# Kernel optimization log

Measured on AMD Instinct MI355X. Metric: run time of the kernel, lower is better.

Reference implementation:

```python
import jax, jax.numpy as jnp
import numpy as np

N = 20000      # nodes
E = 640000     # edges
FIN = 256
FQK = 256


def setup_inputs() -> dict:
    key = jax.random.key(0)
    kx, ks, kd, kw = jax.random.split(key, 4)
    x = jax.random.normal(kx, (N, FIN), dtype=jnp.float32)
    # src must be sorted (original scatter_softmax assumes grouped index);
    # force last element to N-1 so nbatches == N as in batch[-1]+1.
    src = jnp.sort(jax.random.randint(ks, (E,), 0, N))
    src = src.at[-1].set(N - 1)
    dest = jax.random.randint(kd, (E,), 0, N)
    ei = jnp.stack([src, dest]).astype(jnp.int64)
    # nn.Linear(Fin, 2*Fqk, bias=False) weight: [2*Fqk, Fin]
    bound = 1.0 / np.sqrt(FIN)
    W = jax.random.uniform(kw, (2 * FQK, FIN), dtype=jnp.float32,
                           minval=-bound, maxval=bound)
    return {"x": x, "ei": ei, "W": W}


def reference(x, ei, W):
    src, dest = ei[0], ei[1]
    n_nodes = x.shape[0]
    scaling = FQK ** -0.5
    qk = x @ W.T                      # [N, 2*Fqk]
    q, k = jnp.split(qk, 2, axis=-1)  # each [N, Fqk]
    q = q * scaling
    # per-edge dot product: (q[src] . k[dest])  -> [E]
    aw = jnp.einsum('ef,ef->e', q[src], k[dest])
    # scatter softmax over edges grouped by src node (raw exp, as original)
    ex = jnp.exp(aw)
    expsum = jax.ops.segment_sum(ex, src, num_segments=n_nodes)  # [N]
    return ex / expsum[src]
```

## Files before the change

kernel.cpp:

```cpp
#include <hip/hip_runtime.h>
#include <cmath>

#define FIN 256
#define FQK 256
#define SCALING 0.0625f
#define MAX_SEG 256

typedef __bf16 bf16_t;
typedef bf16_t bf16x8 __attribute__((ext_vector_type(8)));
typedef float  f32x4  __attribute__((ext_vector_type(4)));

__device__ __forceinline__ unsigned short f2bf(float f) {
    unsigned int u = __float_as_uint(f);
    u += 0x7FFFu + ((u >> 16) & 1u);
    return (unsigned short)(u >> 16);
}
__device__ __forceinline__ float bf_lo(unsigned int w) { return __uint_as_float(w << 16); }
__device__ __forceinline__ float bf_hi(unsigned int w) { return __uint_as_float(w & 0xFFFF0000u); }

__device__ __forceinline__ bf16x8 cvt8(float4 a, float4 b) {
    bf16x8 r;
    r[0] = (bf16_t)a.x; r[1] = (bf16_t)a.y; r[2] = (bf16_t)a.z; r[3] = (bf16_t)a.w;
    r[4] = (bf16_t)b.x; r[5] = (bf16_t)b.y; r[6] = (bf16_t)b.z; r[7] = (bf16_t)b.w;
    return r;
}

__global__ __launch_bounds__(256) void m_seg_kernel(const float* __restrict__ W,
                                                    unsigned short* __restrict__ Mb,
                                                    const int* __restrict__ src,
                                                    int* __restrict__ seg, int N, int E) {
    const int b = blockIdx.x;
    if (b < FIN) {
        const int f = b;
        const int g = threadIdx.x;
        const float* __restrict__ Wq = W;
        const float* __restrict__ Wk = W + FQK * FIN;
        float acc = 0.f;
#pragma unroll 8
        for (int c = 0; c < FQK; ++c)
            acc += Wq[c * FIN + f] * Wk[c * FIN + g];
        Mb[f * FIN + g] = f2bf(acc * SCALING);
    } else {
        const int n = (b - FIN) * 256 + threadIdx.x;
        if (n > N) return;
        int lo = 0, hi = E;
        while (lo < hi) {
            const int mid = (lo + hi) >> 1;
            if (src[mid] < n) lo = mid + 1; else hi = mid;
        }
        seg[n] = lo;
    }
}

__global__ __launch_bounds__(256) void gemm_y_kernel(const float* __restrict__ x,
                                                     const unsigned short* __restrict__ Mb,
                                                     unsigned short* __restrict__ y, int N) {
    const int t    = threadIdx.x;
    const int wv   = t >> 6;
    const int lane = t & 63;
    const int q    = lane >> 4;
    const int m16  = lane & 15;
    const int n0   = blockIdx.x * 16;
    const int f0   = wv * 64;

    const int row  = n0 + m16;
    const int rowc = row < N ? row : N - 1;
    const float* __restrict__ xr = x + (size_t)rowc * FIN;

    f32x4 acc[4] = {};

#pragma unroll
    for (int kc = 0; kc < FIN; kc += 32) {
        const float4 a0 = *(const float4*)(xr + kc + q * 8);
        const float4 a1 = *(const float4*)(xr + kc + q * 8 + 4);
        const bf16x8 af = cvt8(a0, a1);
#pragma unroll
        for (int ft = 0; ft < 4; ++ft) {
            const int f = f0 + ft * 16 + m16;
            union { uint4 u; bf16x8 v; } bu;
            bu.u = *(const uint4*)(Mb + (size_t)f * FIN + kc + q * 8);
            acc[ft] = __builtin_amdgcn_mfma_f32_16x16x32_bf16(af, bu.v, acc[ft], 0, 0, 0);
        }
    }

#pragma unroll
    for (int r = 0; r < 4; ++r) {
        const int n = n0 + q * 4 + r;
        if (n < N) {
#pragma unroll
            for (int ft = 0; ft < 4; ++ft)
                y[(size_t)n * FIN + f0 + ft * 16 + m16] = f2bf(acc[ft][r]);
        }
    }
}

__device__ __forceinline__ float dot8(uint4 qv, float4 xa, float4 xb) {
    return bf_lo(qv.x) * xa.x + bf_hi(qv.x) * xa.y
         + bf_lo(qv.y) * xa.z + bf_hi(qv.y) * xa.w
         + bf_lo(qv.z) * xb.x + bf_hi(qv.z) * xb.y
         + bf_lo(qv.w) * xb.z + bf_hi(qv.w) * xb.w;
}

__global__ __launch_bounds__(256) void node_edge_kernel(const float* __restrict__ x,
                                                        const unsigned short* __restrict__ y,
                                                        const int* __restrict__ dest,
                                                        const int* __restrict__ seg,
                                                        float* __restrict__ out, int N) {
    __shared__ float exlds[4][MAX_SEG];

    const int w    = threadIdx.x >> 6;
    const int lane = threadIdx.x & 63;
    const int n    = blockIdx.x * 4 + w;
    const int g    = lane >> 3;
    const int j    = lane & 7;

    int   s0 = 0, cnt = 0;
    float inv = 0.f;

    if (n < N) {
        s0  = seg[n];
        cnt = seg[n + 1] - s0;
    }

    if (cnt > 0) {
        float4 xf[8];
        const float* __restrict__ xr = x + (size_t)n * FIN + j * 32;
#pragma unroll
        for (int u = 0; u < 8; ++u) xf[u] = *(const float4*)(xr + u * 4);

        float sum = 0.f;
        const int nit = (cnt + 7) >> 3;
        for (int it = 0; it < nit; ++it) {
            const int i = it * 8 + g;
            if (i < cnt) {
                const int d = dest[s0 + i];
                const uint4* __restrict__ yr =
                    (const uint4*)(y + (size_t)d * FIN) + j * 4;
                const uint4 q0 = yr[0];
                const uint4 q1 = yr[1];
                const uint4 q2 = yr[2];
                const uint4 q3 = yr[3];
                float acc = dot8(q0, xf[0], xf[1]) + dot8(q1, xf[2], xf[3])
                          + dot8(q2, xf[4], xf[5]) + dot8(q3, xf[6], xf[7]);
                acc += __shfl_xor(acc, 1, 64);
                acc += __shfl_xor(acc, 2, 64);
                acc += __shfl_xor(acc, 4, 64);
                const float ex = __expf(acc);
                sum += ex;
                if (j == 0 && i < MAX_SEG) exlds[w][i] = ex;
            }
        }
        sum += __shfl_xor(sum, 8, 64);
        sum += __shfl_xor(sum, 16, 64);
        sum += __shfl_xor(sum, 32, 64);
        inv = 1.0f / sum;
    }

    __syncthreads();

    if (cnt > 0) {
        const int lim = cnt < MAX_SEG ? cnt : MAX_SEG;
        for (int i = lane; i < lim; i += 64)
            out[s0 + i] = exlds[w][i] * inv;
    }
}

extern "C" void kernel_launch(void* const* d_in, const int* in_sizes, int n_in,
                              void* d_out, int out_size, void* d_ws, size_t ws_size,
                              hipStream_t stream) {
    const float* x  = (const float*)d_in[0];
    const int*   ei = (const int*)d_in[1];
    const float* W  = (const float*)d_in[2];
    float* out = (float*)d_out;

    const int N = in_sizes[0] / FIN;
    const int E = in_sizes[1] / 2;

    unsigned short* Mb  = (unsigned short*)d_ws;
    unsigned short* y   = Mb + (size_t)FIN * FIN;
    int*            seg = (int*)(y + (size_t)N * FIN);

    const int segBlocks = (N + 256) / 256;
    m_seg_kernel<<<FIN + segBlocks, 256, 0, stream>>>(W, Mb, ei, seg, N, E);

    gemm_y_kernel<<<(N + 15) / 16, 256, 0, stream>>>(x, Mb, y, N);

    node_edge_kernel<<<(N + 3) / 4, 256, 0, stream>>>(x, y, ei + E, seg, out, N);
}
```

Baseline: 160.9 us.

## Pre-swizzle M into MFMA fragment layout, stage x in LDS, prefetch edge rows

M is now written already arranged in MFMA B-fragment order, so each lane's B load in the GEMM is contiguous. The GEMM block grows to 32 rows: x is converted to bf16 once into padded LDS and each B fragment feeds two MFMAs. The edge loop software-pipelines the gather of the next edge's y row while the current dot product is computed, to hide gather latency. In exchange the GEMM uses more LDS and registers and launches fewer blocks, and the prefetch adds register pressure in the edge kernel.

Measured after the change: 137.1 us. 14.8% less time.

```diff
diff --git a/kernel.cpp b/kernel.cpp
--- a/kernel.cpp
+++ b/kernel.cpp
@@ -5,6 +5,7 @@
 #define FQK 256
 #define SCALING 0.0625f
 #define MAX_SEG 256
+#define ASTRIDE 264
 
 typedef __bf16 bf16_t;
 typedef bf16_t bf16x8 __attribute__((ext_vector_type(8)));
@@ -26,20 +27,22 @@
 }
 
 __global__ __launch_bounds__(256) void m_seg_kernel(const float* __restrict__ W,
-                                                    unsigned short* __restrict__ Mb,
+                                                    unsigned short* __restrict__ MbF,
                                                     const int* __restrict__ src,
                                                     int* __restrict__ seg, int N, int E) {
     const int b = blockIdx.x;
     if (b < FIN) {
         const int f = b;
-        const int g = threadIdx.x;
+        const int k = threadIdx.x;
         const float* __restrict__ Wq = W;
         const float* __restrict__ Wk = W + FQK * FIN;
         float acc = 0.f;
 #pragma unroll 8
         for (int c = 0; c < FQK; ++c)
-            acc += Wq[c * FIN + f] * Wk[c * FIN + g];
-        Mb[f * FIN + g] = f2bf(acc * SCALING);
+            acc += Wq[c * FIN + f] * Wk[c * FIN + k];
+        const int ft  = f >> 4, m16 = f & 15;
+        const int kcI = k >> 5, q = (k >> 3) & 3, e = k & 7;
+        MbF[(size_t)(((kcI * 16 + ft) * 64 + q * 16 + m16) * 8 + e)] = f2bf(acc * SCALING);
     } else {
         const int n = (b - FIN) * 256 + threadIdx.x;
         if (n > N) return;
@@ -53,43 +56,66 @@
 }
 
 __global__ __launch_bounds__(256) void gemm_y_kernel(const float* __restrict__ x,
-                                                     const unsigned short* __restrict__ Mb,
+                                                     const unsigned short* __restrict__ MbF,
                                                      unsigned short* __restrict__ y, int N) {
+    __shared__ unsigned short sA[32 * ASTRIDE];
+
     const int t    = threadIdx.x;
     const int wv   = t >> 6;
     const int lane = t & 63;
     const int q    = lane >> 4;
     const int m16  = lane & 15;
-    const int n0   = blockIdx.x * 16;
+    const int n0   = blockIdx.x * 32;
     const int f0   = wv * 64;
 
-    const int row  = n0 + m16;
-    const int rowc = row < N ? row : N - 1;
-    const float* __restrict__ xr = x + (size_t)rowc * FIN;
-
-    f32x4 acc[4] = {};
+    {
+        const int srow = t >> 3;
+        const int scol = (t & 7) * 32;
+        const int n    = n0 + srow;
+        const int nc   = n < N ? n : N - 1;
+        const float* __restrict__ xp = x + (size_t)nc * FIN + scol;
+        unsigned short* __restrict__ sp = &sA[srow * ASTRIDE + scol];
+#pragma unroll
+        for (int u = 0; u < 4; ++u) {
+            const float4 a = *(const float4*)(xp + u * 8);
+            const float4 b = *(const float4*)(xp + u * 8 + 4);
+            *(bf16x8*)(sp + u * 8) = cvt8(a, b);
+        }
+    }
+    __syncthreads();
+
+    f32x4 acc[2][4] = {};
 
 #pragma unroll
     for (int kc = 0; kc < FIN; kc += 32) {
-        const float4 a0 = *(const float4*)(xr + kc + q * 8);
-        const float4 a1 = *(const float4*)(xr + kc + q * 8 + 4);
-        const bf16x8 af = cvt8(a0, a1);
+        bf16x8 afrag[2];
+#pragma unroll
+        for (int mt = 0; mt < 2; ++mt)
+            afrag[mt] = *(const bf16x8*)&sA[(mt * 16 + m16) * ASTRIDE + kc + q * 8];
+
+        const unsigned short* __restrict__ bp =
+            MbF + (size_t)(((kc >> 5) * 16 + (f0 >> 4)) * 64 + lane) * 8;
 #pragma unroll
         for (int ft = 0; ft < 4; ++ft) {
-            const int f = f0 + ft * 16 + m16;
             union { uint4 u; bf16x8 v; } bu;
-            bu.u = *(const uint4*)(Mb + (size_t)f * FIN + kc + q * 8);
-            acc[ft] = __builtin_amdgcn_mfma_f32_16x16x32_bf16(af, bu.v, acc[ft], 0, 0, 0);
-        }
-    }
-
-#pragma unroll
-    for (int r = 0; r < 4; ++r) {
-        const int n = n0 + q * 4 + r;
-        if (n < N) {
-#pragma unroll
-            for (int ft = 0; ft < 4; ++ft)
-                y[(size_t)n * FIN + f0 + ft * 16 + m16] = f2bf(acc[ft][r]);
+            bu.u = *(const uint4*)(bp + ft * 512);
+#pragma unroll
+            for (int mt = 0; mt < 2; ++mt)
+                acc[mt][ft] = __builtin_amdgcn_mfma_f32_16x16x32_bf16(afrag[mt], bu.v,
+                                                                     acc[mt][ft], 0, 0, 0);
+        }
+    }
+
+#pragma unroll
+    for (int mt = 0; mt < 2; ++mt) {
+#pragma unroll
+        for (int r = 0; r < 4; ++r) {
+            const int n = n0 + mt * 16 + q * 4 + r;
+            if (n < N) {
+#pragma unroll
+                for (int ft = 0; ft < 4; ++ft)
+                    y[(size_t)n * FIN + f0 + ft * 16 + m16] = f2bf(acc[mt][ft][r]);
+            }
         }
     }
 }
@@ -130,18 +156,28 @@
 
         float sum = 0.f;
         const int nit = (cnt + 7) >> 3;
+
+        uint4 c0, c1, c2, c3;
+        bool vc = g < cnt;
+        if (vc) {
+            const int d = dest[s0 + g];
+            const uint4* __restrict__ yr = (const uint4*)(y + (size_t)d * FIN) + j * 4;
+            c0 = yr[0]; c1 = yr[1]; c2 = yr[2]; c3 = yr[3];
+        }
+
         for (int it = 0; it < nit; ++it) {
-            const int i = it * 8 + g;
-            if (i < cnt) {
-                const int d = dest[s0 + i];
-                const uint4* __restrict__ yr =
-                    (const uint4*)(y + (size_t)d * FIN) + j * 4;
-                const uint4 q0 = yr[0];
-                const uint4 q1 = yr[1];
-                const uint4 q2 = yr[2];
-                const uint4 q3 = yr[3];
-                float acc = dot8(q0, xf[0], xf[1]) + dot8(q1, xf[2], xf[3])
-                          + dot8(q2, xf[4], xf[5]) + dot8(q3, xf[6], xf[7]);
+            const int i   = it * 8 + g;
+            const int inx = i + 8;
+            const bool vn = inx < cnt;
+            uint4 p0, p1, p2, p3;
+            if (vn) {
+                const int d = dest[s0 + inx];
+                const uint4* __restrict__ yr = (const uint4*)(y + (size_t)d * FIN) + j * 4;
+                p0 = yr[0]; p1 = yr[1]; p2 = yr[2]; p3 = yr[3];
+            }
+            if (vc) {
+                float acc = dot8(c0, xf[0], xf[1]) + dot8(c1, xf[2], xf[3])
+                          + dot8(c2, xf[4], xf[5]) + dot8(c3, xf[6], xf[7]);
                 acc += __shfl_xor(acc, 1, 64);
                 acc += __shfl_xor(acc, 2, 64);
                 acc += __shfl_xor(acc, 4, 64);
@@ -149,6 +185,7 @@
                 sum += ex;
                 if (j == 0 && i < MAX_SEG) exlds[w][i] = ex;
             }
+            c0 = p0; c1 = p1; c2 = p2; c3 = p3; vc = vn;
         }
         sum += __shfl_xor(sum, 8, 64);
         sum += __shfl_xor(sum, 16, 64);
@@ -176,14 +213,14 @@
     const int N = in_sizes[0] / FIN;
     const int E = in_sizes[1] / 2;
 
-    unsigned short* Mb  = (unsigned short*)d_ws;
-    unsigned short* y   = Mb + (size_t)FIN * FIN;
+    unsigned short* MbF = (unsigned short*)d_ws;
+    unsigned short* y   = MbF + (size_t)FIN * FIN;
     int*            seg = (int*)(y + (size_t)N * FIN);
 
     const int segBlocks = (N + 256) / 256;
-    m_seg_kernel<<<FIN + segBlocks, 256, 0, stream>>>(W, Mb, ei, seg, N, E);
-
-    gemm_y_kernel<<<(N + 15) / 16, 256, 0, stream>>>(x, Mb, y, N);
+    m_seg_kernel<<<FIN + segBlocks, 256, 0, stream>>>(W, MbF, ei, seg, N, E);
+
+    gemm_y_kernel<<<(N + 31) / 32, 256, 0, stream>>>(x, MbF, y, N);
 
     node_edge_kernel<<<(N + 3) / 4, 256, 0, stream>>>(x, y, ei + E, seg, out, N);
 }
```
